# Performance work log

Measured on AMD Instinct MI355X. Metric: run time of the kernel, lower is better.

The kernel has to match this reference:

```python
import jax, jax.numpy as jnp
import numpy as np

D = 1024      # d_model
H = 16        # n_heads
M = 64        # n_memories
DK = D // H   # head dim
EPS = 1e-5    # LayerNorm eps


def setup_inputs() -> dict:
    key = jax.random.key(0)
    ks = jax.random.split(key, 16)
    B, N = 4, 1024
    s = 0.02
    return {
        "queries": jax.random.normal(ks[0], (B, N, D), jnp.float32),
        "keys": jax.random.normal(ks[1], (B, N, D), jnp.float32),
        "values": jax.random.normal(ks[2], (B, N, D), jnp.float32),
        "attention_mask": jax.random.randint(ks[3], (B, 1, 1, N), 0, 2, dtype=jnp.int32),
        "Wq": jax.random.normal(ks[4], (D, D), jnp.float32) * s,
        "bq": jnp.zeros((D,), jnp.float32),
        "Wk": jax.random.normal(ks[5], (D, D), jnp.float32) * s,
        "bk": jnp.zeros((D,), jnp.float32),
        "Wv": jax.random.normal(ks[6], (D, D), jnp.float32) * s,
        "bv": jnp.zeros((D,), jnp.float32),
        "Wo": jax.random.normal(ks[7], (D, D), jnp.float32) * s,
        "bo": jnp.zeros((D,), jnp.float32),
        "m_k": jax.random.normal(ks[8], (1, M, D), jnp.float32) * 0.01,
        "m_v": jax.random.normal(ks[9], (1, M, D), jnp.float32) * 0.01,
        "gamma": jnp.ones((D,), jnp.float32),
        "beta": jnp.zeros((D,), jnp.float32),
    }


def _layer_norm(x, gamma, beta):
    mu = jnp.mean(x, axis=-1, keepdims=True)
    var = jnp.var(x, axis=-1, keepdims=True)
    return (x - mu) * jax.lax.rsqrt(var + EPS) * gamma + beta


def reference(queries, keys, values, attention_mask,
              Wq, bq, Wk, bk, Wv, bv, Wo, bo, m_k, m_v, gamma, beta):
    B, Nq, _ = queries.shape
    Nk = keys.shape[1]
    scale = 1.0 / np.sqrt(DK)

    # projections (torch Linear: x @ W.T + b)
    q = (queries @ Wq.T + bq).reshape(B, Nq, H, DK).transpose(0, 2, 1, 3)  # b h nq d

    # memory-augmented K/V (memory tokens scaled as in the source)
    k_full = jnp.concatenate(
        [keys @ Wk.T + bk, jnp.broadcast_to(m_k * np.sqrt(DK), (B, M, D))], axis=1)
    v_full = jnp.concatenate(
        [values @ Wv.T + bv, jnp.broadcast_to(m_v * np.sqrt(M), (B, M, D))], axis=1)
    k = k_full.reshape(B, Nk + M, H, DK).transpose(0, 2, 1, 3)  # b h nk+m d
    v = v_full.reshape(B, Nk + M, H, DK).transpose(0, 2, 1, 3)  # b h nk+m d

    scores = jnp.einsum('bhqd,bhkd->bhqk', q, k) * scale  # [B,H,Nq,Nk+M]

    # partial masking: only the first Nk (non-memory) columns are maskable
    mask = jnp.concatenate(
        [attention_mask.astype(bool),
         jnp.zeros((B, 1, 1, M), dtype=bool)], axis=-1)
    scores = jnp.where(mask, -jnp.inf, scores)

    p_attn = jax.nn.softmax(scores, axis=-1)  # dropout p=0.0 -> identity
    out = jnp.einsum('bhqk,bhkd->bhqd', p_attn, v)
    out = out.transpose(0, 2, 1, 3).reshape(B, Nq, D)
    out = out @ Wo.T + bo

    # residual + LayerNorm (outer dropout is identity at p=0.0)
    return _layer_norm(queries + out, gamma, beta)
```

## Files before the change

### kernel.cpp

```cpp
#include <hip/hip_runtime.h>


typedef __bf16 bf16;
typedef __bf16 bf16x8 __attribute__((ext_vector_type(8)));
typedef __bf16 bf16x4 __attribute__((ext_vector_type(4)));
typedef float  f32x4  __attribute__((ext_vector_type(4)));

#define NSEQ 1024
#define NKV  1088
#define DMODEL 1024

struct CvtArgs { const float* s[7]; };

__global__ __launch_bounds__(256) void cvt_bf16(CvtArgs c, bf16* __restrict__ dst)
{
    size_t e = ((size_t)blockIdx.x * 256 + threadIdx.x) * 8;
    const float* s;
    if (e < ((size_t)3 << 22)) {
        s = c.s[e >> 22] + (e & 0x3FFFFF);
    } else {
        size_t wq = e - ((size_t)3 << 22);
        s = c.s[3 + (wq >> 20)] + (wq & 0xFFFFF);
    }
    f32x4 a = *(const f32x4*)s;
    f32x4 b = *(const f32x4*)(s + 4);
    bf16x8 o;
    for (int i = 0; i < 4; i++) { o[i] = (bf16)a[i]; o[4 + i] = (bf16)b[i]; }
    *(bf16x8*)&dst[e] = o;
}

typedef __attribute__((address_space(1))) void gas_void;
typedef __attribute__((address_space(3))) void las_void;

__device__ __forceinline__ void gload16(const bf16* g, bf16* l)
{
    __builtin_amdgcn_global_load_lds((gas_void*)g, (las_void*)l, 16, 0, 0);
}

struct GemmArgsB {
    const bf16* A;
    const bf16* W;
    const float* bias;
    bf16* C;
    int osK;
    int vt;
};

__global__ __launch_bounds__(256, 3) void gemm128_lds(GemmArgsB g0, GemmArgsB g1,
                                                      GemmArgsB g2)
{
    const GemmArgsB g = (blockIdx.z == 0) ? g0 : (blockIdx.z == 1) ? g1 : g2;
    __shared__ bf16 As[128][32];
    __shared__ bf16 Bs[128][32];
    const int t = threadIdx.x;
    const int lane = t & 63, w = t >> 6;
    const int qi = lane & 15, qq = lane >> 4;
    const int wrow = (w >> 1) * 64, wcol = (w & 1) * 64;
    const int bm = blockIdx.y * 128, bn = blockIdx.x * 128;

    const int srow = w * 32 + (lane >> 2);
    const int scol = (lane & 3) * 8;
    const bf16* Ag = g.A + (size_t)(bm + srow) * DMODEL + scol;
    const bf16* Wg = g.W + (size_t)(bn + srow) * DMODEL + scol;
    bf16* Al = &As[w * 32][0];
    bf16* Bl = &Bs[w * 32][0];

    f32x4 acc[4][4] = {};

#define STAGE(kt)                                                             \
    do {                                                                      \
        gload16(Ag + (kt),                 Al);                               \
        gload16(Ag + (kt) + 16 * DMODEL,   Al + 16 * 32);                     \
        gload16(Wg + (kt),                 Bl);                               \
        gload16(Wg + (kt) + 16 * DMODEL,   Bl + 16 * 32);                     \
    } while (0)

    STAGE(0);
    for (int kt = 0; kt < DMODEL; kt += 32) {
        __syncthreads();
        bf16x8 a[4], b[4];
        for (int i = 0; i < 4; i++)
            a[i] = *(const bf16x8*)&As[wrow + i * 16 + qi][qq * 8];
        for (int j = 0; j < 4; j++)
            b[j] = *(const bf16x8*)&Bs[wcol + j * 16 + qi][qq * 8];
        __syncthreads();
        if (kt + 32 < DMODEL) STAGE(kt + 32);
        for (int i = 0; i < 4; i++)
            for (int j = 0; j < 4; j++)
                acc[i][j] = __builtin_amdgcn_mfma_f32_16x16x32_bf16(
                    a[i], b[j], acc[i][j], 0, 0, 0);
    }
#undef STAGE

    for (int i = 0; i < 4; i++)
        for (int j = 0; j < 4; j++) {
            int row0 = bm + wrow + i * 16 + qq * 4;
            int col  = bn + wcol + j * 16 + qi;
            float bcol = g.bias[col];
            if (g.vt) {
                bf16x4 v;
                for (int r = 0; r < 4; r++) v[r] = (bf16)(acc[i][j][r] + bcol);
                size_t off = ((size_t)((row0 >> 10) * 16 + (col >> 6)) * 64 + (col & 63))
                           * NKV + (row0 & 1023);
                *(bf16x4*)&g.C[off] = v;
            } else {
                for (int r = 0; r < 4; r++) {
                    int row = row0 + r;
                    size_t off = (size_t)(row >> 10) * g.osK
                               + (size_t)(row & 1023) * DMODEL + col;
                    g.C[off] = (bf16)(acc[i][j][r] + bcol);
                }
            }
        }
}

struct GemmArgs {
    const void* A;
    const float* W;
    const float* bias;
    bf16* C;
    int osK;
    int vt;
};

template<bool ABF>
__global__ __launch_bounds__(256, 2) void gemm128(GemmArgs g0, GemmArgs g1, GemmArgs g2)
{
    const GemmArgs g = (blockIdx.z == 0) ? g0 : (blockIdx.z == 1) ? g1 : g2;
    __shared__ bf16 As[128][44];
    __shared__ bf16 Bs[128][44];
    const int t = threadIdx.x;
    const int lane = t & 63, w = t >> 6;
    const int qi = lane & 15, qq = lane >> 4;
    const int wrow = (w >> 1) * 64, wcol = (w & 1) * 64;
    const int bm = blockIdx.y * 128, bn = blockIdx.x * 128;
    const int sr = t >> 1, sc = (t & 1) * 16;

    f32x4 acc[4][4] = {};

    f32x4 pa[4];
    bf16x8 pab[2];
    f32x4 pw[4];

    const float* Wp = g.W + (size_t)(bn + sr) * DMODEL + sc;
    const float* Af = (const float*)g.A + (size_t)(bm + sr) * DMODEL + sc;
    const bf16*  Ab = (const bf16*)g.A + (size_t)(bm + sr) * DMODEL + sc;

#define LOAD_TILES(kt)                                                        \
    do {                                                                      \
        if (ABF) {                                                            \
            pab[0] = *(const bf16x8*)(Ab + (kt));                             \
            pab[1] = *(const bf16x8*)(Ab + (kt) + 8);                         \
        } else {                                                              \
            pa[0] = *(const f32x4*)(Af + (kt));                               \
            pa[1] = *(const f32x4*)(Af + (kt) + 4);                           \
            pa[2] = *(const f32x4*)(Af + (kt) + 8);                           \
            pa[3] = *(const f32x4*)(Af + (kt) + 12);                          \
        }                                                                     \
        pw[0] = *(const f32x4*)(Wp + (kt));                                   \
        pw[1] = *(const f32x4*)(Wp + (kt) + 4);                               \
        pw[2] = *(const f32x4*)(Wp + (kt) + 8);                               \
        pw[3] = *(const f32x4*)(Wp + (kt) + 12);                              \
    } while (0)

#define STORE_TILES()                                                         \
    do {                                                                      \
        if (ABF) {                                                            \
            *(bf16x8*)&As[sr][sc]     = pab[0];                               \
            *(bf16x8*)&As[sr][sc + 8] = pab[1];                               \
        } else {                                                              \
            bf16x8 v0, v1;                                                    \
            for (int i = 0; i < 4; i++) {                                     \
                v0[i] = (bf16)pa[0][i]; v0[4 + i] = (bf16)pa[1][i];           \
                v1[i] = (bf16)pa[2][i]; v1[4 + i] = (bf16)pa[3][i];           \
            }                                                                 \
            *(bf16x8*)&As[sr][sc]     = v0;                                   \
            *(bf16x8*)&As[sr][sc + 8] = v1;                                   \
        }                                                                     \
        {                                                                     \
            bf16x8 u0, u1;                                                    \
            for (int i = 0; i < 4; i++) {                                     \
                u0[i] = (bf16)pw[0][i]; u0[4 + i] = (bf16)pw[1][i];           \
                u1[i] = (bf16)pw[2][i]; u1[4 + i] = (bf16)pw[3][i];           \
            }                                                                 \
            *(bf16x8*)&Bs[sr][sc]     = u0;                                   \
            *(bf16x8*)&Bs[sr][sc + 8] = u1;                                   \
        }                                                                     \
    } while (0)

    LOAD_TILES(0);
    STORE_TILES();
    __syncthreads();

    for (int kt = 0; kt < DMODEL; kt += 32) {
        const bool more = (kt + 32) < DMODEL;
        if (more) LOAD_TILES(kt + 32);
        bf16x8 a[4], b[4];
        for (int i = 0; i < 4; i++)
            a[i] = *(const bf16x8*)&As[wrow + i * 16 + qi][qq * 8];
        for (int j = 0; j < 4; j++)
            b[j] = *(const bf16x8*)&Bs[wcol + j * 16 + qi][qq * 8];
        for (int i = 0; i < 4; i++)
            for (int j = 0; j < 4; j++)
                acc[i][j] = __builtin_amdgcn_mfma_f32_16x16x32_bf16(a[i], b[j], acc[i][j], 0, 0, 0);
        if (more) {
            __syncthreads();
            STORE_TILES();
            __syncthreads();
        }
    }
#undef LOAD_TILES
#undef STORE_TILES

    for (int i = 0; i < 4; i++)
        for (int j = 0; j < 4; j++) {
            int row0 = bm + wrow + i * 16 + qq * 4;
            int col  = bn + wcol + j * 16 + qi;
            float bcol = g.bias[col];
            if (g.vt) {
                bf16x4 v;
                for (int r = 0; r < 4; r++) v[r] = (bf16)(acc[i][j][r] + bcol);
                size_t off = ((size_t)((row0 >> 10) * 16 + (col >> 6)) * 64 + (col & 63))
                           * NKV + (row0 & 1023);
                *(bf16x4*)&g.C[off] = v;
            } else {
                for (int r = 0; r < 4; r++) {
                    int row = row0 + r;
                    size_t off = (size_t)(row >> 10) * g.osK
                               + (size_t)(row & 1023) * DMODEL + col;
                    g.C[off] = (bf16)(acc[i][j][r] + bcol);
                }
            }
        }
}

__global__ void fill_mem(const float* __restrict__ mk, const float* __restrict__ mv,
                         bf16* __restrict__ K, bf16* __restrict__ Vt)
{
    int i = blockIdx.x * 256 + threadIdx.x;
    int b = i >> 16, md = i & 65535;
    int m = md >> 10, dcol = md & 1023;
    K[(size_t)b * (NKV * DMODEL) + (size_t)(NSEQ + m) * DMODEL + dcol]
        = (bf16)(mk[md] * 8.0f);
    Vt[((size_t)b * 1024 + dcol) * NKV + NSEQ + m] = (bf16)(mv[md] * 8.0f);
}

__global__ __launch_bounds__(256) void attn_flash(const bf16* Q,
        const bf16* __restrict__ K, const bf16* __restrict__ Vt,
        const int* __restrict__ mask, bf16* O)
{
    __shared__ bf16  sK[64][72];
    __shared__ bf16  sV[64][72];
    __shared__ bf16  sP[4][16][72];
    __shared__ float sM[NKV];
    const int t = threadIdx.x, lane = t & 63, w = t >> 6;
    const int bh = blockIdx.y, b = bh >> 4, h = bh & 15;
    const int q0 = blockIdx.x * 64;
    const int sr = t >> 2, sc = (t & 3) * 16;
    const int qi = lane & 15, qq = lane >> 4;

    for (int j = t; j < NKV; j += 256)
        sM[j] = (j < NSEQ && mask[b * NSEQ + j] != 0) ? -3.0e38f : 0.0f;

    const size_t qbase = (size_t)(b * NSEQ + q0 + w * 16 + qi) * DMODEL
                       + h * 64 + qq * 8;
    bf16x8 qa0 = *(const bf16x8*)&Q[qbase];
    bf16x8 qa1 = *(const bf16x8*)&Q[qbase + 32];
    for (int i = 0; i < 8; i++) {
        qa0[i] = (bf16)((float)qa0[i] * 0.125f);
        qa1[i] = (bf16)((float)qa1[i] * 0.125f);
    }

    const bf16* kbase = K + (size_t)(b * NKV + sr) * DMODEL + h * 64 + sc;
    const bf16* vbase = Vt + ((size_t)bh * 64 + sr) * NKV + sc;

    bf16x8 pk0, pk1, pv0, pv1;
#define LOAD_KV(jt)                                                           \
    do {                                                                      \
        const bf16* kp = kbase + (size_t)(jt) * 64 * DMODEL;                  \
        pk0 = *(const bf16x8*)kp;                                             \
        pk1 = *(const bf16x8*)(kp + 8);                                       \
        const bf16* vp = vbase + (jt) * 64;                                   \
        pv0 = *(const bf16x8*)vp;                                             \
        pv1 = *(const bf16x8*)(vp + 8);                                       \
    } while (0)
#define STORE_KV()                                                            \
    do {                                                                      \
        *(bf16x8*)&sK[sr][sc]     = pk0;                                      \
        *(bf16x8*)&sK[sr][sc + 8] = pk1;                                      \
        *(bf16x8*)&sV[sr][sc]     = pv0;                                      \
        *(bf16x8*)&sV[sr][sc + 8] = pv1;                                      \
    } while (0)

    LOAD_KV(0);
    STORE_KV();

    float m_i[4], l_i[4];
    f32x4 oacc[4] = {};
    for (int r = 0; r < 4; r++) { m_i[r] = -3.0e38f; l_i[r] = 0.f; }

    for (int jt = 0; jt < 17; jt++) {
        const int j0 = jt * 64;
        __syncthreads();
        const bool more = jt < 16;
        if (more) LOAD_KV(jt + 1);

        f32x4 s[4];
        for (int g = 0; g < 4; g++) {
            bf16x8 b0 = *(const bf16x8*)&sK[g * 16 + qi][qq * 8];
            bf16x8 b1 = *(const bf16x8*)&sK[g * 16 + qi][32 + qq * 8];
            f32x4 a = {};
            a = __builtin_amdgcn_mfma_f32_16x16x32_bf16(qa0, b0, a, 0, 0, 0);
            a = __builtin_amdgcn_mfma_f32_16x16x32_bf16(qa1, b1, a, 0, 0, 0);
            float msk = sM[j0 + g * 16 + qi];
            for (int r = 0; r < 4; r++) s[g][r] = a[r] + msk;
        }
        float alpha[4];
        for (int r = 0; r < 4; r++) {
            float rm = fmaxf(fmaxf(s[0][r], s[1][r]), fmaxf(s[2][r], s[3][r]));
            for (int o = 1; o < 16; o <<= 1) rm = fmaxf(rm, __shfl_xor(rm, o, 64));
            float mnew = fmaxf(m_i[r], rm);
            alpha[r] = __expf(m_i[r] - mnew);
            m_i[r] = mnew;
            float rs = 0.f;
            for (int g = 0; g < 4; g++) {
                float p = __expf(s[g][r] - mnew);
                s[g][r] = p;
                rs += p;
            }
            for (int o = 1; o < 16; o <<= 1) rs += __shfl_xor(rs, o, 64);
            l_i[r] = l_i[r] * alpha[r] + rs;
        }
        for (int g = 0; g < 4; g++)
            for (int r = 0; r < 4; r++) {
                sP[w][qq * 4 + r][g * 16 + qi] = (bf16)s[g][r];
                oacc[g][r] *= alpha[r];
            }
        bf16x8 af0 = *(const bf16x8*)&sP[w][qi][qq * 8];
        bf16x8 af1 = *(const bf16x8*)&sP[w][qi][32 + qq * 8];
        for (int g = 0; g < 4; g++) {
            bf16x8 v0 = *(const bf16x8*)&sV[g * 16 + qi][qq * 8];
            bf16x8 v1 = *(const bf16x8*)&sV[g * 16 + qi][32 + qq * 8];
            oacc[g] = __builtin_amdgcn_mfma_f32_16x16x32_bf16(af0, v0, oacc[g], 0, 0, 0);
            oacc[g] = __builtin_amdgcn_mfma_f32_16x16x32_bf16(af1, v1, oacc[g], 0, 0, 0);
        }
        __syncthreads();
        if (more) STORE_KV();
    }
#undef LOAD_KV
#undef STORE_KV

    float inv[4];
    for (int r = 0; r < 4; r++) inv[r] = 1.0f / l_i[r];
    for (int g = 0; g < 4; g++)
        for (int r = 0; r < 4; r++) {
            int row = q0 + w * 16 + qq * 4 + r;
            int col = h * 64 + g * 16 + qi;
            O[(size_t)(b * NSEQ + row) * DMODEL + col] = (bf16)(oacc[g][r] * inv[r]);
        }
}

__global__ __launch_bounds__(256) void residual_ln(const float* __restrict__ X,
        const bf16* __restrict__ Y, const float* __restrict__ gamma,
        const float* __restrict__ beta, float* __restrict__ out)
{
    __shared__ float red[8];
    int row = blockIdx.x, t = threadIdx.x;
    size_t base = (size_t)row * DMODEL + t * 4;
    f32x4  xv = *(const f32x4*)&X[base];
    bf16x4 yv = *(const bf16x4*)&Y[base];
    float s[4], sum = 0.f, sq = 0.f;
    for (int i = 0; i < 4; i++) {
        s[i] = xv[i] + (float)yv[i];
        sum += s[i]; sq += s[i] * s[i];
    }
    for (int o = 32; o; o >>= 1) { sum += __shfl_xor(sum, o, 64); sq += __shfl_xor(sq, o, 64); }
    if ((t & 63) == 0) { red[t >> 6] = sum; red[4 + (t >> 6)] = sq; }
    __syncthreads();
    sum = red[0] + red[1] + red[2] + red[3];
    sq  = red[4] + red[5] + red[6] + red[7];
    float mean = sum * (1.0f / DMODEL);
    float var  = sq  * (1.0f / DMODEL) - mean * mean;
    float rstd = rsqrtf(var + 1e-5f);
    f32x4 gv = *(const f32x4*)&gamma[t * 4];
    f32x4 bv = *(const f32x4*)&beta[t * 4];
    f32x4 ov;
    for (int i = 0; i < 4; i++)
        ov[i] = (s[i] - mean) * rstd * gv[i] + bv[i];
    *(f32x4*)&out[base] = ov;
}

extern "C" void kernel_launch(void* const* d_in, const int* in_sizes, int n_in,
                              void* d_out, int out_size, void* d_ws, size_t ws_size,
                              hipStream_t stream)
{
    const float* queries = (const float*)d_in[0];
    const float* keys    = (const float*)d_in[1];
    const float* values  = (const float*)d_in[2];
    const int*   amask   = (const int*)d_in[3];
    const float* Wq = (const float*)d_in[4];  const float* bq = (const float*)d_in[5];
    const float* Wk = (const float*)d_in[6];  const float* bk = (const float*)d_in[7];
    const float* Wv = (const float*)d_in[8];  const float* bv = (const float*)d_in[9];
    const float* Wo = (const float*)d_in[10]; const float* bo = (const float*)d_in[11];
    const float* mk = (const float*)d_in[12]; const float* mv = (const float*)d_in[13];
    const float* gamma = (const float*)d_in[14]; const float* beta = (const float*)d_in[15];
    float* out = (float*)d_out;

    bf16* Qb = (bf16*)(out + (size_t)2 * 1024 * 1024);
    const size_t SB  = (size_t)NSEQ * DMODEL;
    const size_t KVB = (size_t)NKV * DMODEL;
    dim3 gb(256);

    const size_t need_r10 = (2 * 4 * KVB + 3 * 4 * SB + 4 * SB) * sizeof(bf16);

    if (ws_size >= need_r10) {
        bf16* Kb = (bf16*)d_ws;
        bf16* Vt = Kb + 4 * KVB;
        bf16* Ab = Vt + 4 * KVB;
        bf16* Wb = Ab + 12 * SB;
        bf16* PR = Ab;

        CvtArgs ca;
        ca.s[0] = queries; ca.s[1] = keys; ca.s[2] = values;
        ca.s[3] = Wq; ca.s[4] = Wk; ca.s[5] = Wv; ca.s[6] = Wo;
        cvt_bf16<<<dim3(8192), gb, 0, stream>>>(ca, Ab);

        GemmArgsB gq{Ab,           Wb,           bq, Qb, (int)SB,  0};
        GemmArgsB gk{Ab + 4 * SB,  Wb + SB,      bk, Kb, (int)KVB, 0};
        GemmArgsB gv{Ab + 8 * SB,  Wb + 2 * SB,  bv, Vt, 0,        1};
        gemm128_lds<<<dim3(8, 32, 3), gb, 0, stream>>>(gq, gk, gv);
        fill_mem<<<dim3(1024), gb, 0, stream>>>(mk, mv, Kb, Vt);
        attn_flash<<<dim3(16, 64), gb, 0, stream>>>(Qb, Kb, Vt, amask, Qb);
        GemmArgsB go{Qb, Wb + 3 * SB, bo, PR, (int)SB, 0};
        gemm128_lds<<<dim3(8, 32, 1), gb, 0, stream>>>(go, go, go);
        residual_ln<<<dim3(4096), gb, 0, stream>>>(queries, PR, gamma, beta, out);
    } else if (ws_size >= (size_t)2 * 4 * KVB * sizeof(bf16)) {
        bf16* Kb = (bf16*)d_ws;
        bf16* Vt = Kb + 4 * KVB;
        bf16* PR = Kb;

        GemmArgs gq{queries, Wq, bq, Qb, (int)SB,  0};
        GemmArgs gk{keys,    Wk, bk, Kb, (int)KVB, 0};
        GemmArgs gv{values,  Wv, bv, Vt, 0,        1};
        gemm128<false><<<dim3(8, 32, 3), gb, 0, stream>>>(gq, gk, gv);
        fill_mem<<<dim3(1024), gb, 0, stream>>>(mk, mv, Kb, Vt);
        attn_flash<<<dim3(16, 64), gb, 0, stream>>>(Qb, Kb, Vt, amask, Qb);
        GemmArgs go{Qb, Wo, bo, PR, (int)SB, 0};
        gemm128<true><<<dim3(8, 32, 1), gb, 0, stream>>>(go, go, go);
        residual_ln<<<dim3(4096), gb, 0, stream>>>(queries, PR, gamma, beta, out);
    } else {
        bf16* Kb = (bf16*)d_ws;
        bf16* Vt = Kb + KVB;
        bf16* PR = Kb;

        GemmArgs gq{queries, Wq, bq, Qb, (int)SB, 0};
        gemm128<false><<<dim3(8, 32, 1), gb, 0, stream>>>(gq, gq, gq);
        for (int b = 0; b < 4; b++) {
            GemmArgs gk{keys   + b * SB, Wk, bk, Kb, 0, 0};
            GemmArgs gv{values + b * SB, Wv, bv, Vt, 0, 1};
            gemm128<false><<<dim3(8, 8, 2), gb, 0, stream>>>(gk, gv, gv);
            fill_mem<<<dim3(256), gb, 0, stream>>>(mk, mv, Kb, Vt);
            attn_flash<<<dim3(16, 16), gb, 0, stream>>>(Qb + b * SB, Kb, Vt,
                                                        amask + b * NSEQ, Qb + b * SB);
            GemmArgs go{Qb + b * SB, Wo, bo, PR, 0, 0};
            gemm128<true><<<dim3(8, 8, 1), gb, 0, stream>>>(go, go, go);
            residual_ln<<<dim3(1024), gb, 0, stream>>>(queries + b * SB, PR,
                                                       gamma, beta, out + b * SB);
        }
    }
}
```

Measured before the change: 265.5 us.

## Widen attention KV tile to 128, read V from global, fuse memory fill into prep

```diff
diff --git a/kernel.cpp b/kernel.cpp
--- a/kernel.cpp
+++ b/kernel.cpp
@@ -8,25 +8,38 @@
 
 #define NSEQ 1024
 #define NKV  1088
+#define NKVP 1152
 #define DMODEL 1024
 
-struct CvtArgs { const float* s[7]; };
-
-__global__ __launch_bounds__(256) void cvt_bf16(CvtArgs c, bf16* __restrict__ dst)
-{
-    size_t e = ((size_t)blockIdx.x * 256 + threadIdx.x) * 8;
-    const float* s;
-    if (e < ((size_t)3 << 22)) {
-        s = c.s[e >> 22] + (e & 0x3FFFFF);
+struct CvtArgs { const float* s[7]; const float* mk; const float* mv; };
+
+__global__ __launch_bounds__(256) void prep(CvtArgs c, bf16* __restrict__ dst,
+                                            bf16* __restrict__ Kb,
+                                            bf16* __restrict__ Vt)
+{
+    int blk = blockIdx.x;
+    if (blk < 8192) {
+        size_t e = ((size_t)blk * 256 + threadIdx.x) * 8;
+        const float* s;
+        if (e < ((size_t)3 << 22)) {
+            s = c.s[e >> 22] + (e & 0x3FFFFF);
+        } else {
+            size_t wq = e - ((size_t)3 << 22);
+            s = c.s[3 + (wq >> 20)] + (wq & 0xFFFFF);
+        }
+        f32x4 a = *(const f32x4*)s;
+        f32x4 b = *(const f32x4*)(s + 4);
+        bf16x8 o;
+        for (int i = 0; i < 4; i++) { o[i] = (bf16)a[i]; o[4 + i] = (bf16)b[i]; }
+        *(bf16x8*)&dst[e] = o;
     } else {
-        size_t wq = e - ((size_t)3 << 22);
-        s = c.s[3 + (wq >> 20)] + (wq & 0xFFFFF);
-    }
-    f32x4 a = *(const f32x4*)s;
-    f32x4 b = *(const f32x4*)(s + 4);
-    bf16x8 o;
-    for (int i = 0; i < 4; i++) { o[i] = (bf16)a[i]; o[4 + i] = (bf16)b[i]; }
-    *(bf16x8*)&dst[e] = o;
+        int i = (blk - 8192) * 256 + threadIdx.x;
+        int b = i >> 16, md = i & 65535;
+        int m = md >> 10, dcol = md & 1023;
+        Kb[(size_t)b * (NKV * DMODEL) + (size_t)(NSEQ + m) * DMODEL + dcol]
+            = (bf16)(c.mk[md] * 8.0f);
+        Vt[((size_t)b * 1024 + dcol) * NKV + NSEQ + m] = (bf16)(c.mv[md] * 8.0f);
+    }
 }
 
 typedef __attribute__((address_space(1))) void gas_void;
@@ -249,18 +262,25 @@
         const bf16* __restrict__ K, const bf16* __restrict__ Vt,
         const int* __restrict__ mask, bf16* O)
 {
-    __shared__ bf16  sK[64][72];
-    __shared__ bf16  sV[64][72];
+    __shared__ bf16  sK[128][72];
     __shared__ bf16  sP[4][16][72];
-    __shared__ float sM[NKV];
+    __shared__ float sM[NKVP];
     const int t = threadIdx.x, lane = t & 63, w = t >> 6;
-    const int bh = blockIdx.y, b = bh >> 4, h = bh & 15;
-    const int q0 = blockIdx.x * 64;
-    const int sr = t >> 2, sc = (t & 3) * 16;
+    int bh, q0;
+    if (gridDim.y == 64) {
+        int lin = blockIdx.y * 16 + blockIdx.x;
+        bh = ((lin & 7) << 3) | ((lin >> 3) & 7);
+        q0 = (lin >> 6) * 64;
+    } else {
+        bh = blockIdx.y;
+        q0 = blockIdx.x * 64;
+    }
+    const int b = bh >> 4, h = bh & 15;
     const int qi = lane & 15, qq = lane >> 4;
 
-    for (int j = t; j < NKV; j += 256)
-        sM[j] = (j < NSEQ && mask[b * NSEQ + j] != 0) ? -3.0e38f : 0.0f;
+    for (int j = t; j < NKVP; j += 256)
+        sM[j] = (j < NSEQ) ? ((mask[b * NSEQ + j] != 0) ? -3.0e38f : 0.0f)
+                           : (j < NKV ? 0.0f : -3.0e38f);
 
     const size_t qbase = (size_t)(b * NSEQ + q0 + w * 16 + qi) * DMODEL
                        + h * 64 + qq * 8;
@@ -271,42 +291,42 @@
         qa1[i] = (bf16)((float)qa1[i] * 0.125f);
     }
 
-    const bf16* kbase = K + (size_t)(b * NKV + sr) * DMODEL + h * 64 + sc;
-    const bf16* vbase = Vt + ((size_t)bh * 64 + sr) * NKV + sc;
-
-    bf16x8 pk0, pk1, pv0, pv1;
-#define LOAD_KV(jt)                                                           \
+    const int ksr = t >> 1, ksc = (t & 1) * 32;
+    const bf16* vbase = Vt + (size_t)bh * 64 * NKV;
+    bf16x8 pk[4];
+#define LOAD_K(jt)                                                            \
     do {                                                                      \
-        const bf16* kp = kbase + (size_t)(jt) * 64 * DMODEL;                  \
-        pk0 = *(const bf16x8*)kp;                                             \
-        pk1 = *(const bf16x8*)(kp + 8);                                       \
-        const bf16* vp = vbase + (jt) * 64;                                   \
-        pv0 = *(const bf16x8*)vp;                                             \
-        pv1 = *(const bf16x8*)(vp + 8);                                       \
+        int kr = (jt) * 128 + ksr;                                            \
+        if (kr > NKV - 1) kr = NKV - 1;                                       \
+        const bf16* kp = K + ((size_t)b * NKV + kr) * DMODEL + h * 64 + ksc;  \
+        pk[0] = *(const bf16x8*)kp;                                           \
+        pk[1] = *(const bf16x8*)(kp + 8);                                     \
+        pk[2] = *(const bf16x8*)(kp + 16);                                    \
+        pk[3] = *(const bf16x8*)(kp + 24);                                    \
     } while (0)
-#define STORE_KV()                                                            \
+#define STORE_K()                                                             \
     do {                                                                      \
-        *(bf16x8*)&sK[sr][sc]     = pk0;                                      \
-        *(bf16x8*)&sK[sr][sc + 8] = pk1;                                      \
-        *(bf16x8*)&sV[sr][sc]     = pv0;                                      \
-        *(bf16x8*)&sV[sr][sc + 8] = pv1;                                      \
+        *(bf16x8*)&sK[ksr][ksc]      = pk[0];                                 \
+        *(bf16x8*)&sK[ksr][ksc + 8]  = pk[1];                                 \
+        *(bf16x8*)&sK[ksr][ksc + 16] = pk[2];                                 \
+        *(bf16x8*)&sK[ksr][ksc + 24] = pk[3];                                 \
     } while (0)
 
-    LOAD_KV(0);
-    STORE_KV();
+    LOAD_K(0);
+    STORE_K();
 
     float m_i[4], l_i[4];
     f32x4 oacc[4] = {};
     for (int r = 0; r < 4; r++) { m_i[r] = -3.0e38f; l_i[r] = 0.f; }
 
-    for (int jt = 0; jt < 17; jt++) {
-        const int j0 = jt * 64;
+    for (int jt = 0; jt < 9; jt++) {
+        const int j0 = jt * 128;
         __syncthreads();
-        const bool more = jt < 16;
-        if (more) LOAD_KV(jt + 1);
-
-        f32x4 s[4];
-        for (int g = 0; g < 4; g++) {
+        const bool more = jt < 8;
+        if (more) LOAD_K(jt + 1);
+
+        f32x4 s[8];
+        for (int g = 0; g < 8; g++) {
             bf16x8 b0 = *(const bf16x8*)&sK[g * 16 + qi][qq * 8];
             bf16x8 b1 = *(const bf16x8*)&sK[g * 16 + qi][32 + qq * 8];
             f32x4 a = {};
@@ -317,13 +337,14 @@
         }
         float alpha[4];
         for (int r = 0; r < 4; r++) {
-            float rm = fmaxf(fmaxf(s[0][r], s[1][r]), fmaxf(s[2][r], s[3][r]));
+            float rm = fmaxf(fmaxf(fmaxf(s[0][r], s[1][r]), fmaxf(s[2][r], s[3][r])),
+                             fmaxf(fmaxf(s[4][r], s[5][r]), fmaxf(s[6][r], s[7][r])));
             for (int o = 1; o < 16; o <<= 1) rm = fmaxf(rm, __shfl_xor(rm, o, 64));
             float mnew = fmaxf(m_i[r], rm);
             alpha[r] = __expf(m_i[r] - mnew);
             m_i[r] = mnew;
             float rs = 0.f;
-            for (int g = 0; g < 4; g++) {
+            for (int g = 0; g < 8; g++) {
                 float p = __expf(s[g][r] - mnew);
                 s[g][r] = p;
                 rs += p;
@@ -332,23 +353,34 @@
             l_i[r] = l_i[r] * alpha[r] + rs;
         }
         for (int g = 0; g < 4; g++)
-            for (int r = 0; r < 4; r++) {
-                sP[w][qq * 4 + r][g * 16 + qi] = (bf16)s[g][r];
-                oacc[g][r] *= alpha[r];
+            for (int r = 0; r < 4; r++) oacc[g][r] *= alpha[r];
+
+        for (int half = 0; half < 2; half++) {
+            const int kc = j0 + half * 64;
+            if (kc >= NKV) break;
+            int c0 = kc + qq * 8;       if (c0 > NKV - 8) c0 = NKV - 8;
+            int c1 = kc + 32 + qq * 8;  if (c1 > NKV - 8) c1 = NKV - 8;
+            bf16x8 vf[4][2];
+            for (int g = 0; g < 4; g++) {
+                const bf16* vrow = vbase + (size_t)(g * 16 + qi) * NKV;
+                vf[g][0] = *(const bf16x8*)&vrow[c0];
+                vf[g][1] = *(const bf16x8*)&vrow[c1];
             }
-        bf16x8 af0 = *(const bf16x8*)&sP[w][qi][qq * 8];
-        bf16x8 af1 = *(const bf16x8*)&sP[w][qi][32 + qq * 8];
-        for (int g = 0; g < 4; g++) {
-            bf16x8 v0 = *(const bf16x8*)&sV[g * 16 + qi][qq * 8];
-            bf16x8 v1 = *(const bf16x8*)&sV[g * 16 + qi][32 + qq * 8];
-            oacc[g] = __builtin_amdgcn_mfma_f32_16x16x32_bf16(af0, v0, oacc[g], 0, 0, 0);
-            oacc[g] = __builtin_amdgcn_mfma_f32_16x16x32_bf16(af1, v1, oacc[g], 0, 0, 0);
+            for (int g = 0; g < 4; g++)
+                for (int r = 0; r < 4; r++)
+                    sP[w][qq * 4 + r][g * 16 + qi] = (bf16)s[half * 4 + g][r];
+            bf16x8 af0 = *(const bf16x8*)&sP[w][qi][qq * 8];
+            bf16x8 af1 = *(const bf16x8*)&sP[w][qi][32 + qq * 8];
+            for (int g = 0; g < 4; g++) {
+                oacc[g] = __builtin_amdgcn_mfma_f32_16x16x32_bf16(af0, vf[g][0], oacc[g], 0, 0, 0);
+                oacc[g] = __builtin_amdgcn_mfma_f32_16x16x32_bf16(af1, vf[g][1], oacc[g], 0, 0, 0);
+            }
         }
         __syncthreads();
-        if (more) STORE_KV();
-    }
-#undef LOAD_KV
-#undef STORE_KV
+        if (more) STORE_K();
+    }
+#undef LOAD_K
+#undef STORE_K
 
     float inv[4];
     for (int r = 0; r < 4; r++) inv[r] = 1.0f / l_i[r];
@@ -423,13 +455,13 @@
         CvtArgs ca;
         ca.s[0] = queries; ca.s[1] = keys; ca.s[2] = values;
         ca.s[3] = Wq; ca.s[4] = Wk; ca.s[5] = Wv; ca.s[6] = Wo;
-        cvt_bf16<<<dim3(8192), gb, 0, stream>>>(ca, Ab);
+        ca.mk = mk; ca.mv = mv;
+        prep<<<dim3(8192 + 1024), gb, 0, stream>>>(ca, Ab, Kb, Vt);
 
         GemmArgsB gq{Ab,           Wb,           bq, Qb, (int)SB,  0};
         GemmArgsB gk{Ab + 4 * SB,  Wb + SB,      bk, Kb, (int)KVB, 0};
         GemmArgsB gv{Ab + 8 * SB,  Wb + 2 * SB,  bv, Vt, 0,        1};
         gemm128_lds<<<dim3(8, 32, 3), gb, 0, stream>>>(gq, gk, gv);
-        fill_mem<<<dim3(1024), gb, 0, stream>>>(mk, mv, Kb, Vt);
         attn_flash<<<dim3(16, 64), gb, 0, stream>>>(Qb, Kb, Vt, amask, Qb);
         GemmArgsB go{Qb, Wb + 3 * SB, bo, PR, (int)SB, 0};
         gemm128_lds<<<dim3(8, 32, 1), gb, 0, stream>>>(go, go, go);
```

Result: slower. 296.3 us (+11.6%).
